# Kernel tuning notes

Hardware: AMD Instinct MI355X
Metric: run time of the kernel (lower is better)

Reference implementation:

```python
import jax, jax.numpy as jnp
import numpy as np

LN_EPS = 1e-5

def _layernorm(x, scale, bias):
    mu = jnp.mean(x, axis=-1, keepdims=True)
    var = jnp.var(x, axis=-1, keepdims=True)
    return (x - mu) * jax.lax.rsqrt(var + LN_EPS) * scale + bias

def setup_inputs() -> dict:
    T, node_num, num_nodes, E, C = 4, 10000, 50000, 256, 128
    key = jax.random.key(0)
    ks = jax.random.split(key, 12)
    s = lambda fan_in: 1.0 / np.sqrt(fan_in)
    return {
        "x": jax.random.normal(ks[0], (T * node_num, E), jnp.float32),
        "batched_x": jax.random.normal(ks[1], (num_nodes, E), jnp.float32),
        "indices": jax.random.randint(ks[2], (T, node_num), 0, num_nodes, jnp.int32),
        "ln_d_scale": jnp.ones((E,), jnp.float32),
        "ln_d_bias": jnp.zeros((E,), jnp.float32),
        "W1_d": jax.random.normal(ks[3], (E, 2 * E), jnp.float32) * s(E),
        "b1_d": jnp.zeros((2 * E,), jnp.float32),
        "W2_d": jax.random.normal(ks[4], (2 * E, C), jnp.float32) * s(2 * E),
        "b2_d": jnp.zeros((C,), jnp.float32),
        "ln_u_scale": jnp.ones((C,), jnp.float32),
        "ln_u_bias": jnp.zeros((C,), jnp.float32),
        "W1_u": jax.random.normal(ks[5], (C, 2 * C), jnp.float32) * s(C),
        "b1_u": jnp.zeros((2 * C,), jnp.float32),
        "W2_u": jax.random.normal(ks[6], (2 * C, E), jnp.float32) * s(2 * C),
        "b2_u": jnp.zeros((E,), jnp.float32),
    }

def reference(x, batched_x, indices, ln_d_scale, ln_d_bias, W1_d, b1_d, W2_d, b2_d,
              ln_u_scale, ln_u_bias, W1_u, b1_u, W2_u, b2_u):
    T, node_num = indices.shape
    num_nodes, E = batched_x.shape
    xr = x.reshape(T, node_num, E)
    # _to_entire: per-step scatter-add of active-node embeddings into the full node table
    def scatter_one(xi, idx):
        return jnp.zeros((num_nodes, E), x.dtype).at[idx].add(xi)
    ta = jax.vmap(scatter_one)(xr, indices)          # [T, num_nodes, E]
    inp = ta + batched_x[None]                        # broadcast entire features
    h = _layernorm(inp, ln_d_scale, ln_d_bias)
    h = jax.nn.gelu(h @ W1_d + b1_d, approximate=False) @ W2_d + b2_d  # [T, num_nodes, C]
    # _from_entire: gather each step's active nodes back, concat, LN + MLP up
    g = jnp.take_along_axis(h, indices[..., None], axis=1)  # [T, node_num, C]
    g = g.reshape(T * node_num, -1)
    g = _layernorm(g, ln_u_scale, ln_u_bias)
    out = jax.nn.gelu(g @ W1_u + b1_u, approximate=False) @ W2_u + b2_u  # [T*node_num, E]
    return out
```

## Files before the change

kernel.cpp:

```cpp
#include <hip/hip_runtime.h>
#include <math.h>

#define T_STEPS   4
#define NODE_NUM  10000
#define NUM_NODES 50000
#define E         256
#define TWO_E     512
#define CC        128
#define TWO_C     256
#define ROWS      32
#define NROWS_ALL (T_STEPS * NODE_NUM)
#define MAX_SLOTS 20000

typedef short bf16x8 __attribute__((ext_vector_type(8)));
typedef float f32x4  __attribute__((ext_vector_type(4)));

#define MFMA16(a, b, c) __builtin_amdgcn_mfma_f32_16x16x32_bf16((a), (b), (c), 0, 0, 0)

static __device__ unsigned short g_wt[294912];
static __device__ int g_cnt[T_STEPS * NUM_NODES];
static __device__ int g_slot[T_STEPS * NUM_NODES];
static __device__ int g_nslots;
static __device__ int g_dup[NROWS_ALL];
static __device__ int g_ndup0;

__device__ __forceinline__ float geluf(float v) {
    float p = v * (1.5957691216057308f + 0.07135481282636226f * v * v);
    return v / (1.0f + __expf(-p));
}

__device__ __forceinline__ unsigned short f2bf(float f) {
    unsigned int u = __builtin_bit_cast(unsigned int, f);
    u += 0x7fffu + ((u >> 16) & 1u);
    return (unsigned short)(u >> 16);
}

__global__ void prep_weights(float* __restrict__ ctable,
                             const float* __restrict__ W1d, const float* __restrict__ W2d,
                             const float* __restrict__ W1u, const float* __restrict__ W2u) {
    int i = blockIdx.x * 256 + threadIdx.x;
    if (i == 0) { g_nslots = 0; g_ndup0 = 0; }
    if (i < T_STEPS * NUM_NODES) g_cnt[i] = 0;
    {
        float4 z = make_float4(0.f, 0.f, 0.f, 0.f);
        float4* ct4 = reinterpret_cast<float4*>(ctable);
        for (int j = i; j < MAX_SLOTS * E / 4; j += 200704) ct4[j] = z;
    }
    if (i < 131072) {
        int n = i >> 8, k = i & 255;
        g_wt[i] = f2bf(W1d[(size_t)k * TWO_E + n]);
    }
    if (i < 65536) {
        int n = i >> 9, k = i & 511;
        g_wt[131072 + i] = f2bf(W2d[(size_t)k * CC + n]);
    }
    if (i < 32768) {
        int n = i >> 7, k = i & 127;
        g_wt[196608 + i] = f2bf(W1u[(size_t)k * TWO_C + n]);
    }
    if (i < 65536) {
        int n = i >> 8, k = i & 255;
        g_wt[229376 + i] = f2bf(W2u[(size_t)k * E + n]);
    }
}

__global__ void count_kernel(const int* __restrict__ indices) {
    int gr = blockIdx.x * 256 + threadIdx.x;
    if (gr < NROWS_ALL) {
        int t = gr / NODE_NUM;
        atomicAdd(&g_cnt[t * NUM_NODES + indices[gr]], 1);
    }
}

__global__ void index_prep_kernel(const int* __restrict__ indices) {
    int i = blockIdx.x * 256 + threadIdx.x;
    if (i < T_STEPS * NUM_NODES && g_cnt[i] >= 2)
        g_slot[i] = atomicAdd(&g_nslots, 1);
    if (i < NROWS_ALL) {
        int t = i / NODE_NUM;
        if (g_cnt[t * NUM_NODES + indices[i]] >= 2) {
            int p = atomicAdd(&g_ndup0, 1);
            g_dup[p] = i;
        }
    }
}

__global__ void scatter_list_kernel(float* __restrict__ ctable,
                                    const float* __restrict__ x,
                                    const int* __restrict__ indices) {
    int nd = g_ndup0;
    for (int e = blockIdx.x; e < nd; e += gridDim.x) {
        int gr = g_dup[e];
        int t = gr / NODE_NUM;
        int slot = g_slot[t * NUM_NODES + indices[gr]];
        atomicAdd(&ctable[(size_t)slot * E + threadIdx.x],
                  x[(size_t)gr * E + threadIdx.x]);
    }
}

__global__ __launch_bounds__(256, 3)
void mlp_kernel(const float* __restrict__ ctable,
                const float* __restrict__ x,
                const float* __restrict__ batched_x,
                const int* __restrict__ indices,
                const float* __restrict__ lnd_s, const float* __restrict__ lnd_b,
                const float* __restrict__ b1d, const float* __restrict__ b2d,
                const float* __restrict__ lnu_s, const float* __restrict__ lnu_b,
                const float* __restrict__ b1u, const float* __restrict__ b2u,
                float* __restrict__ out,
                int grLim) {
    __shared__ __align__(16) unsigned char smem[50176];
    __shared__ const float* rptr[ROWS];
    __shared__ int    ridx[ROWS];

    float*          Xf  = (float*)smem;
    unsigned short* Xs  = (unsigned short*)(smem + 33280);
    unsigned short* H1  = (unsigned short*)smem;
    float*          H2f = (float*)(smem + 33280);
    unsigned short* H2b = (unsigned short*)smem;
    unsigned short* G1  = (unsigned short*)(smem + 8704);

    const unsigned short* w1t  = g_wt;
    const unsigned short* w2t  = g_wt + 131072;
    const unsigned short* w1ut = g_wt + 196608;
    const unsigned short* w2ut = g_wt + 229376;

    const int tid = threadIdx.x;
    const int w = tid >> 6, lane = tid & 63;
    const int l16 = lane & 15, quad = lane >> 4;
    const int grb = blockIdx.x * ROWS;

    if (tid < ROWS) {
        int gr = grb + tid;
        if (gr >= grLim) gr = grLim - 1;
        int t = gr / NODE_NUM;
        int key = t * NUM_NODES + indices[gr];
        ridx[tid] = indices[gr];
        rptr[tid] = (g_cnt[key] > 1)
            ? (ctable + (size_t)g_slot[key] * E)
            : (x + (size_t)gr * E);
    }
    __syncthreads();

    #pragma unroll
    for (int it = 0; it < 8; ++it) {
        int v = it * 256 + tid;
        int r = v >> 6;
        int c = (v & 63) * 4;
        float4 tv = *reinterpret_cast<const float4*>(rptr[r] + c);
        float4 bv = *reinterpret_cast<const float4*>(&batched_x[(size_t)ridx[r] * E + c]);
        float4 s; s.x = tv.x + bv.x; s.y = tv.y + bv.y; s.z = tv.z + bv.z; s.w = tv.w + bv.w;
        *reinterpret_cast<float4*>(&Xf[r * 260 + c]) = s;
    }
    __syncthreads();

    {
        int row = tid >> 3, l8 = tid & 7;
        float s = 0.f, sq = 0.f;
        #pragma unroll
        for (int k = 0; k < 32; ++k) {
            float v = Xf[row * 260 + k * 8 + l8];
            s += v; sq += v * v;
        }
        s  += __shfl_xor(s, 1);  s  += __shfl_xor(s, 2);  s  += __shfl_xor(s, 4);
        sq += __shfl_xor(sq, 1); sq += __shfl_xor(sq, 2); sq += __shfl_xor(sq, 4);
        float mu = s * (1.0f / E);
        float var = sq * (1.0f / E) - mu * mu;
        float rs = rsqrtf(var + 1e-5f);
        #pragma unroll
        for (int k = 0; k < 32; ++k) {
            int c = k * 8 + l8;
            float v = (Xf[row * 260 + c] - mu) * rs * lnd_s[c] + lnd_b[c];
            Xs[row * 264 + c] = f2bf(v);
        }
    }
    __syncthreads();

    {
        bf16x8 af[2][8];
        #pragma unroll
        for (int mt = 0; mt < 2; ++mt) {
            const unsigned short* base = Xs + (l16 + 16 * mt) * 264 + quad * 8;
            #pragma unroll
            for (int ks = 0; ks < 8; ++ks)
                af[mt][ks] = *reinterpret_cast<const bf16x8*>(base + ks * 32);
        }
        bf16x8 bbuf[2][8];
        {
            const unsigned short* bp = w1t + (size_t)((w * 8) * 16 + l16) * 256 + quad * 8;
            #pragma unroll
            for (int ks = 0; ks < 8; ++ks)
                bbuf[0][ks] = *reinterpret_cast<const bf16x8*>(bp + ks * 32);
        }
        #pragma unroll
        for (int nt_ = 0; nt_ < 8; ++nt_) {
            const int cb = nt_ & 1, nb = cb ^ 1;
            if (nt_ < 7) {
                const unsigned short* bp =
                    w1t + (size_t)((w * 8 + nt_ + 1) * 16 + l16) * 256 + quad * 8;
                #pragma unroll
                for (int ks = 0; ks < 8; ++ks)
                    bbuf[nb][ks] = *reinterpret_cast<const bf16x8*>(bp + ks * 32);
            }
            int n = (w * 8 + nt_) * 16 + l16;
            f32x4 a0 = {0.f, 0.f, 0.f, 0.f}, a1 = {0.f, 0.f, 0.f, 0.f};
            #pragma unroll
            for (int ks = 0; ks < 8; ++ks) {
                a0 = MFMA16(af[0][ks], bbuf[cb][ks], a0);
                a1 = MFMA16(af[1][ks], bbuf[cb][ks], a1);
            }
            float bias = b1d[n];
            #pragma unroll
            for (int reg = 0; reg < 4; ++reg) {
                int r = quad * 4 + reg;
                H1[r * 520 + n]        = f2bf(geluf(a0[reg] + bias));
                H1[(r + 16) * 520 + n] = f2bf(geluf(a1[reg] + bias));
            }
        }
    }
    __syncthreads();

    {
        f32x4 acc2[2][2];
        #pragma unroll
        for (int i = 0; i < 2; ++i)
            #pragma unroll
            for (int j = 0; j < 2; ++j) acc2[i][j] = (f32x4){0.f, 0.f, 0.f, 0.f};
        bf16x8 afk[2][8];
        #pragma unroll
        for (int mt = 0; mt < 2; ++mt) {
            const unsigned short* base = H1 + (l16 + 16 * mt) * 520 + quad * 8;
            #pragma unroll
            for (int ks = 0; ks < 8; ++ks)
                afk[mt][ks] = *reinterpret_cast<const bf16x8*>(base + ks * 32);
        }
        bf16x8 bbuf[2][8];
        {
            const unsigned short* bp = w2t + (size_t)((w * 2) * 16 + l16) * 512 + quad * 8;
            #pragma unroll
            for (int ks = 0; ks < 8; ++ks)
                bbuf[0][ks] = *reinterpret_cast<const bf16x8*>(bp + ks * 32);
        }
        #pragma unroll
        for (int s = 0; s < 4; ++s) {
            const int nt2 = s & 1;
            const int cb = s & 1, nb = cb ^ 1;
            if (s < 3) {
                const int s1 = s + 1, kh1 = s1 >> 1, nt21 = s1 & 1;
                const unsigned short* bp =
                    w2t + (size_t)((w * 2 + nt21) * 16 + l16) * 512 + kh1 * 256 + quad * 8;
                #pragma unroll
                for (int ks = 0; ks < 8; ++ks)
                    bbuf[nb][ks] = *reinterpret_cast<const bf16x8*>(bp + ks * 32);
            }
            if (s == 2) {
                #pragma unroll
                for (int mt = 0; mt < 2; ++mt) {
                    const unsigned short* base = H1 + (l16 + 16 * mt) * 520 + 256 + quad * 8;
                    #pragma unroll
                    for (int ks = 0; ks < 8; ++ks)
                        afk[mt][ks] = *reinterpret_cast<const bf16x8*>(base + ks * 32);
                }
            }
            #pragma unroll
            for (int ks = 0; ks < 8; ++ks) {
                acc2[nt2][0] = MFMA16(afk[0][ks], bbuf[cb][ks], acc2[nt2][0]);
                acc2[nt2][1] = MFMA16(afk[1][ks], bbuf[cb][ks], acc2[nt2][1]);
            }
        }
        #pragma unroll
        for (int nt2 = 0; nt2 < 2; ++nt2) {
            int n = (w * 2 + nt2) * 16 + l16;
            float bias = b2d[n];
            #pragma unroll
            for (int mt = 0; mt < 2; ++mt)
                #pragma unroll
                for (int reg = 0; reg < 4; ++reg) {
                    int r = mt * 16 + quad * 4 + reg;
                    H2f[r * 132 + n] = acc2[nt2][mt][reg] + bias;
                }
        }
    }
    __syncthreads();

    {
        int row = tid >> 3, l8 = tid & 7;
        float s = 0.f, sq = 0.f;
        #pragma unroll
        for (int k = 0; k < 16; ++k) {
            float v = H2f[row * 132 + k * 8 + l8];
            s += v; sq += v * v;
        }
        s  += __shfl_xor(s, 1);  s  += __shfl_xor(s, 2);  s  += __shfl_xor(s, 4);
        sq += __shfl_xor(sq, 1); sq += __shfl_xor(sq, 2); sq += __shfl_xor(sq, 4);
        float mu = s * (1.0f / CC);
        float var = sq * (1.0f / CC) - mu * mu;
        float rs = rsqrtf(var + 1e-5f);
        #pragma unroll
        for (int k = 0; k < 16; ++k) {
            int c = k * 8 + l8;
            float v = (H2f[row * 132 + c] - mu) * rs * lnu_s[c] + lnu_b[c];
            H2b[row * 136 + c] = f2bf(v);
        }
    }
    __syncthreads();

    {
        bf16x8 af3[2][4];
        #pragma unroll
        for (int mt = 0; mt < 2; ++mt) {
            const unsigned short* base = H2b + (l16 + 16 * mt) * 136 + quad * 8;
            #pragma unroll
            for (int ks = 0; ks < 4; ++ks)
                af3[mt][ks] = *reinterpret_cast<const bf16x8*>(base + ks * 32);
        }
        bf16x8 bbuf[2][4];
        {
            const unsigned short* bp = w1ut + (size_t)((w * 4) * 16 + l16) * 128 + quad * 8;
            #pragma unroll
            for (int ks = 0; ks < 4; ++ks)
                bbuf[0][ks] = *reinterpret_cast<const bf16x8*>(bp + ks * 32);
        }
        #pragma unroll
        for (int nt_ = 0; nt_ < 4; ++nt_) {
            const int cb = nt_ & 1, nb = cb ^ 1;
            if (nt_ < 3) {
                const unsigned short* bp =
                    w1ut + (size_t)((w * 4 + nt_ + 1) * 16 + l16) * 128 + quad * 8;
                #pragma unroll
                for (int ks = 0; ks < 4; ++ks)
                    bbuf[nb][ks] = *reinterpret_cast<const bf16x8*>(bp + ks * 32);
            }
            int n = (w * 4 + nt_) * 16 + l16;
            f32x4 a0 = {0.f, 0.f, 0.f, 0.f}, a1 = {0.f, 0.f, 0.f, 0.f};
            #pragma unroll
            for (int ks = 0; ks < 4; ++ks) {
                a0 = MFMA16(af3[0][ks], bbuf[cb][ks], a0);
                a1 = MFMA16(af3[1][ks], bbuf[cb][ks], a1);
            }
            float bias = b1u[n];
            #pragma unroll
            for (int reg = 0; reg < 4; ++reg) {
                int r = quad * 4 + reg;
                G1[r * 264 + n]        = f2bf(geluf(a0[reg] + bias));
                G1[(r + 16) * 264 + n] = f2bf(geluf(a1[reg] + bias));
            }
        }
    }
    __syncthreads();

    {
        bf16x8 af4[2][8];
        #pragma unroll
        for (int mt = 0; mt < 2; ++mt) {
            const unsigned short* base = G1 + (l16 + 16 * mt) * 264 + quad * 8;
            #pragma unroll
            for (int ks = 0; ks < 8; ++ks)
                af4[mt][ks] = *reinterpret_cast<const bf16x8*>(base + ks * 32);
        }
        bf16x8 bbuf[2][8];
        {
            const unsigned short* bp = w2ut + (size_t)((w * 4) * 16 + l16) * 256 + quad * 8;
            #pragma unroll
            for (int ks = 0; ks < 8; ++ks)
                bbuf[0][ks] = *reinterpret_cast<const bf16x8*>(bp + ks * 32);
        }
        #pragma unroll
        for (int nt_ = 0; nt_ < 4; ++nt_) {
            const int cb = nt_ & 1, nb = cb ^ 1;
            if (nt_ < 3) {
                const unsigned short* bp =
                    w2ut + (size_t)((w * 4 + nt_ + 1) * 16 + l16) * 256 + quad * 8;
                #pragma unroll
                for (int ks = 0; ks < 8; ++ks)
                    bbuf[nb][ks] = *reinterpret_cast<const bf16x8*>(bp + ks * 32);
            }
            int n = (w * 4 + nt_) * 16 + l16;
            f32x4 a0 = {0.f, 0.f, 0.f, 0.f}, a1 = {0.f, 0.f, 0.f, 0.f};
            #pragma unroll
            for (int ks = 0; ks < 8; ++ks) {
                a0 = MFMA16(af4[0][ks], bbuf[cb][ks], a0);
                a1 = MFMA16(af4[1][ks], bbuf[cb][ks], a1);
            }
            float bias = b2u[n];
            #pragma unroll
            for (int reg = 0; reg < 4; ++reg) {
                int r = quad * 4 + reg;
                int g0 = grb + r, g1 = grb + r + 16;
                if (g0 < grLim) out[(size_t)g0 * E + n] = a0[reg] + bias;
                if (g1 < grLim) out[(size_t)g1 * E + n] = a1[reg] + bias;
            }
        }
    }
}

extern "C" void kernel_launch(void* const* d_in, const int* in_sizes, int n_in,
                              void* d_out, int out_size, void* d_ws, size_t ws_size,
                              hipStream_t stream) {
    const float* x     = (const float*)d_in[0];
    const float* bx    = (const float*)d_in[1];
    const int*   idxp  = (const int*)  d_in[2];
    const float* lnd_s = (const float*)d_in[3];
    const float* lnd_b = (const float*)d_in[4];
    const float* W1d   = (const float*)d_in[5];
    const float* b1d   = (const float*)d_in[6];
    const float* W2d   = (const float*)d_in[7];
    const float* b2d   = (const float*)d_in[8];
    const float* lnu_s = (const float*)d_in[9];
    const float* lnu_b = (const float*)d_in[10];
    const float* W1u   = (const float*)d_in[11];
    const float* b1u   = (const float*)d_in[12];
    const float* W2u   = (const float*)d_in[13];
    const float* b2u   = (const float*)d_in[14];
    float* out = (float*)d_out;
    float* ctable = (float*)d_ws;
    (void)ws_size; (void)in_sizes; (void)n_in; (void)out_size;

    prep_weights<<<784, 256, 0, stream>>>(ctable, W1d, W2d, W1u, W2u);
    count_kernel<<<(NROWS_ALL + 255) / 256, 256, 0, stream>>>(idxp);
    index_prep_kernel<<<784, 256, 0, stream>>>(idxp);
    scatter_list_kernel<<<1024, E, 0, stream>>>(ctable, x, idxp);
    mlp_kernel<<<NROWS_ALL / ROWS, 256, 0, stream>>>(
        ctable, x, bx, idxp, lnd_s, lnd_b, b1d, b2d,
        lnu_s, lnu_b, b1u, b2u, out, NROWS_ALL);
}
```

Before: 318.0 us.

## Process two row tiles per block and prefetch second tile's gather during first

Each MLP block now handles two 32-row tiles, with half as many blocks launched. The second tile's gather of x/ctable plus batched_x is issued into registers while the first tile's later GEMMs run, and its LayerNorm is written to shared memory during the third GEMM. The down LayerNorm now works straight from registers with wave-wide shuffles instead of staging fp32 rows in shared memory. This aims to hide global gather latency behind MFMA work, at the cost of extra register pressure and fewer blocks to fill the GPU.

```diff
diff --git a/kernel.cpp b/kernel.cpp
--- a/kernel.cpp
+++ b/kernel.cpp
@@ -14,6 +14,7 @@
 
 typedef short bf16x8 __attribute__((ext_vector_type(8)));
 typedef float f32x4  __attribute__((ext_vector_type(4)));
+typedef unsigned short u16x4 __attribute__((ext_vector_type(4)));
 
 #define MFMA16(a, b, c) __builtin_amdgcn_mfma_f32_16x16x32_bf16((a), (b), (c), 0, 0, 0)
 
@@ -95,6 +96,275 @@
         int slot = g_slot[t * NUM_NODES + indices[gr]];
         atomicAdd(&ctable[(size_t)slot * E + threadIdx.x],
                   x[(size_t)gr * E + threadIdx.x]);
+    }
+}
+
+__device__ __forceinline__ void gemm1_phase(const unsigned short* Xs, unsigned short* H1,
+                                            const unsigned short* w1t,
+                                            const float* __restrict__ b1d,
+                                            int w, int l16, int quad) {
+    bf16x8 af[2][8];
+    #pragma unroll
+    for (int mt = 0; mt < 2; ++mt) {
+        const unsigned short* base = Xs + (l16 + 16 * mt) * 264 + quad * 8;
+        #pragma unroll
+        for (int ks = 0; ks < 8; ++ks)
+            af[mt][ks] = *reinterpret_cast<const bf16x8*>(base + ks * 32);
+    }
+    bf16x8 bbuf[2][8];
+    {
+        const unsigned short* bp = w1t + (size_t)((w * 8) * 16 + l16) * 256 + quad * 8;
+        #pragma unroll
+        for (int ks = 0; ks < 8; ++ks)
+            bbuf[0][ks] = *reinterpret_cast<const bf16x8*>(bp + ks * 32);
+    }
+    #pragma unroll
+    for (int nt_ = 0; nt_ < 8; ++nt_) {
+        const int cb = nt_ & 1, nb = cb ^ 1;
+        if (nt_ < 7) {
+            const unsigned short* bp =
+                w1t + (size_t)((w * 8 + nt_ + 1) * 16 + l16) * 256 + quad * 8;
+            #pragma unroll
+            for (int ks = 0; ks < 8; ++ks)
+                bbuf[nb][ks] = *reinterpret_cast<const bf16x8*>(bp + ks * 32);
+        }
+        int n = (w * 8 + nt_) * 16 + l16;
+        f32x4 a0 = {0.f, 0.f, 0.f, 0.f}, a1 = {0.f, 0.f, 0.f, 0.f};
+        #pragma unroll
+        for (int ks = 0; ks < 8; ++ks) {
+            a0 = MFMA16(af[0][ks], bbuf[cb][ks], a0);
+            a1 = MFMA16(af[1][ks], bbuf[cb][ks], a1);
+        }
+        float bias = b1d[n];
+        #pragma unroll
+        for (int reg = 0; reg < 4; ++reg) {
+            int r = quad * 4 + reg;
+            H1[r * 520 + n]        = f2bf(geluf(a0[reg] + bias));
+            H1[(r + 16) * 520 + n] = f2bf(geluf(a1[reg] + bias));
+        }
+    }
+}
+
+__device__ __forceinline__ void gemm2_phase(const unsigned short* H1, float* H2f,
+                                            const unsigned short* w2t,
+                                            const float* __restrict__ b2d,
+                                            int w, int l16, int quad) {
+    f32x4 acc2[2][2];
+    #pragma unroll
+    for (int i = 0; i < 2; ++i)
+        #pragma unroll
+        for (int j = 0; j < 2; ++j) acc2[i][j] = (f32x4){0.f, 0.f, 0.f, 0.f};
+    bf16x8 afk[2][8];
+    #pragma unroll
+    for (int mt = 0; mt < 2; ++mt) {
+        const unsigned short* base = H1 + (l16 + 16 * mt) * 520 + quad * 8;
+        #pragma unroll
+        for (int ks = 0; ks < 8; ++ks)
+            afk[mt][ks] = *reinterpret_cast<const bf16x8*>(base + ks * 32);
+    }
+    bf16x8 bbuf[2][8];
+    {
+        const unsigned short* bp = w2t + (size_t)((w * 2) * 16 + l16) * 512 + quad * 8;
+        #pragma unroll
+        for (int ks = 0; ks < 8; ++ks)
+            bbuf[0][ks] = *reinterpret_cast<const bf16x8*>(bp + ks * 32);
+    }
+    #pragma unroll
+    for (int s = 0; s < 4; ++s) {
+        const int nt2 = s & 1;
+        const int cb = s & 1, nb = cb ^ 1;
+        if (s < 3) {
+            const int s1 = s + 1, kh1 = s1 >> 1, nt21 = s1 & 1;
+            const unsigned short* bp =
+                w2t + (size_t)((w * 2 + nt21) * 16 + l16) * 512 + kh1 * 256 + quad * 8;
+            #pragma unroll
+            for (int ks = 0; ks < 8; ++ks)
+                bbuf[nb][ks] = *reinterpret_cast<const bf16x8*>(bp + ks * 32);
+        }
+        if (s == 2) {
+            #pragma unroll
+            for (int mt = 0; mt < 2; ++mt) {
+                const unsigned short* base = H1 + (l16 + 16 * mt) * 520 + 256 + quad * 8;
+                #pragma unroll
+                for (int ks = 0; ks < 8; ++ks)
+                    afk[mt][ks] = *reinterpret_cast<const bf16x8*>(base + ks * 32);
+            }
+        }
+        #pragma unroll
+        for (int ks = 0; ks < 8; ++ks) {
+            acc2[nt2][0] = MFMA16(afk[0][ks], bbuf[cb][ks], acc2[nt2][0]);
+            acc2[nt2][1] = MFMA16(afk[1][ks], bbuf[cb][ks], acc2[nt2][1]);
+        }
+    }
+    #pragma unroll
+    for (int nt2 = 0; nt2 < 2; ++nt2) {
+        int n = (w * 2 + nt2) * 16 + l16;
+        float bias = b2d[n];
+        #pragma unroll
+        for (int mt = 0; mt < 2; ++mt)
+            #pragma unroll
+            for (int reg = 0; reg < 4; ++reg) {
+                int r = mt * 16 + quad * 4 + reg;
+                H2f[r * 132 + n] = acc2[nt2][mt][reg] + bias;
+            }
+    }
+}
+
+__device__ __forceinline__ void lnu_phase(const float* H2f, unsigned short* H2b,
+                                          const float* __restrict__ lnu_s,
+                                          const float* __restrict__ lnu_b, int tid) {
+    int row = tid >> 3, l8 = tid & 7;
+    float s = 0.f, sq = 0.f;
+    #pragma unroll
+    for (int k = 0; k < 16; ++k) {
+        float v = H2f[row * 132 + k * 8 + l8];
+        s += v; sq += v * v;
+    }
+    s  += __shfl_xor(s, 1);  s  += __shfl_xor(s, 2);  s  += __shfl_xor(s, 4);
+    sq += __shfl_xor(sq, 1); sq += __shfl_xor(sq, 2); sq += __shfl_xor(sq, 4);
+    float mu = s * (1.0f / CC);
+    float var = sq * (1.0f / CC) - mu * mu;
+    float rs = rsqrtf(var + 1e-5f);
+    #pragma unroll
+    for (int k = 0; k < 16; ++k) {
+        int c = k * 8 + l8;
+        float v = (H2f[row * 132 + c] - mu) * rs * lnu_s[c] + lnu_b[c];
+        H2b[row * 136 + c] = f2bf(v);
+    }
+}
+
+__device__ __forceinline__ void gemm3_phase(const unsigned short* H2b, unsigned short* G1,
+                                            const unsigned short* w1ut,
+                                            const float* __restrict__ b1u,
+                                            int w, int l16, int quad) {
+    bf16x8 af3[2][4];
+    #pragma unroll
+    for (int mt = 0; mt < 2; ++mt) {
+        const unsigned short* base = H2b + (l16 + 16 * mt) * 136 + quad * 8;
+        #pragma unroll
+        for (int ks = 0; ks < 4; ++ks)
+            af3[mt][ks] = *reinterpret_cast<const bf16x8*>(base + ks * 32);
+    }
+    bf16x8 bbuf[2][4];
+    {
+        const unsigned short* bp = w1ut + (size_t)((w * 4) * 16 + l16) * 128 + quad * 8;
+        #pragma unroll
+        for (int ks = 0; ks < 4; ++ks)
+            bbuf[0][ks] = *reinterpret_cast<const bf16x8*>(bp + ks * 32);
+    }
+    #pragma unroll
+    for (int nt_ = 0; nt_ < 4; ++nt_) {
+        const int cb = nt_ & 1, nb = cb ^ 1;
+        if (nt_ < 3) {
+            const unsigned short* bp =
+                w1ut + (size_t)((w * 4 + nt_ + 1) * 16 + l16) * 128 + quad * 8;
+            #pragma unroll
+            for (int ks = 0; ks < 4; ++ks)
+                bbuf[nb][ks] = *reinterpret_cast<const bf16x8*>(bp + ks * 32);
+        }
+        int n = (w * 4 + nt_) * 16 + l16;
+        f32x4 a0 = {0.f, 0.f, 0.f, 0.f}, a1 = {0.f, 0.f, 0.f, 0.f};
+        #pragma unroll
+        for (int ks = 0; ks < 4; ++ks) {
+            a0 = MFMA16(af3[0][ks], bbuf[cb][ks], a0);
+            a1 = MFMA16(af3[1][ks], bbuf[cb][ks], a1);
+        }
+        float bias = b1u[n];
+        #pragma unroll
+        for (int reg = 0; reg < 4; ++reg) {
+            int r = quad * 4 + reg;
+            G1[r * 264 + n]        = f2bf(geluf(a0[reg] + bias));
+            G1[(r + 16) * 264 + n] = f2bf(geluf(a1[reg] + bias));
+        }
+    }
+}
+
+__device__ __forceinline__ void gemm4_phase(const unsigned short* G1,
+                                            const unsigned short* w2ut,
+                                            const float* __restrict__ b2u,
+                                            float* __restrict__ out,
+                                            int grb, int grLim, int w, int l16, int quad) {
+    bf16x8 af4[2][8];
+    #pragma unroll
+    for (int mt = 0; mt < 2; ++mt) {
+        const unsigned short* base = G1 + (l16 + 16 * mt) * 264 + quad * 8;
+        #pragma unroll
+        for (int ks = 0; ks < 8; ++ks)
+            af4[mt][ks] = *reinterpret_cast<const bf16x8*>(base + ks * 32);
+    }
+    bf16x8 bbuf[2][8];
+    {
+        const unsigned short* bp = w2ut + (size_t)((w * 4) * 16 + l16) * 256 + quad * 8;
+        #pragma unroll
+        for (int ks = 0; ks < 8; ++ks)
+            bbuf[0][ks] = *reinterpret_cast<const bf16x8*>(bp + ks * 32);
+    }
+    #pragma unroll
+    for (int nt_ = 0; nt_ < 4; ++nt_) {
+        const int cb = nt_ & 1, nb = cb ^ 1;
+        if (nt_ < 3) {
+            const unsigned short* bp =
+                w2ut + (size_t)((w * 4 + nt_ + 1) * 16 + l16) * 256 + quad * 8;
+            #pragma unroll
+            for (int ks = 0; ks < 8; ++ks)
+                bbuf[nb][ks] = *reinterpret_cast<const bf16x8*>(bp + ks * 32);
+        }
+        int n = (w * 4 + nt_) * 16 + l16;
+        f32x4 a0 = {0.f, 0.f, 0.f, 0.f}, a1 = {0.f, 0.f, 0.f, 0.f};
+        #pragma unroll
+        for (int ks = 0; ks < 8; ++ks) {
+            a0 = MFMA16(af4[0][ks], bbuf[cb][ks], a0);
+            a1 = MFMA16(af4[1][ks], bbuf[cb][ks], a1);
+        }
+        float bias = b2u[n];
+        #pragma unroll
+        for (int reg = 0; reg < 4; ++reg) {
+            int r = quad * 4 + reg;
+            int g0 = grb + r, g1 = grb + r + 16;
+            if (g0 < grLim) out[(size_t)g0 * E + n] = a0[reg] + bias;
+            if (g1 < grLim) out[(size_t)g1 * E + n] = a1[reg] + bias;
+        }
+    }
+}
+
+__device__ __forceinline__ void stage_gather(float4* stg, const float* const* rptr,
+                                             const int* ridx, const float* __restrict__ bx,
+                                             int base, int w, int c4) {
+    #pragma unroll
+    for (int it = 0; it < 8; ++it) {
+        int r = base + it * 4 + w;
+        float4 tv = *reinterpret_cast<const float4*>(rptr[r] + c4);
+        float4 bv = *reinterpret_cast<const float4*>(&bx[(size_t)ridx[r] * E + c4]);
+        float4 s; s.x = tv.x + bv.x; s.y = tv.y + bv.y; s.z = tv.z + bv.z; s.w = tv.w + bv.w;
+        stg[it] = s;
+    }
+}
+
+__device__ __forceinline__ void lnd_from_regs(const float4* stg, unsigned short* Xs,
+                                              const float* __restrict__ lnd_s,
+                                              const float* __restrict__ lnd_b,
+                                              int w, int c4) {
+    const float4 sc = *reinterpret_cast<const float4*>(lnd_s + c4);
+    const float4 bi = *reinterpret_cast<const float4*>(lnd_b + c4);
+    #pragma unroll
+    for (int it = 0; it < 8; ++it) {
+        const int r = it * 4 + w;
+        float4 a = stg[it];
+        float s  = a.x + a.y + a.z + a.w;
+        float sq = a.x*a.x + a.y*a.y + a.z*a.z + a.w*a.w;
+        #pragma unroll
+        for (int m = 1; m < 64; m <<= 1) {
+            s  += __shfl_xor(s,  m);
+            sq += __shfl_xor(sq, m);
+        }
+        const float mu = s * (1.0f / E);
+        const float rs = rsqrtf(sq * (1.0f / E) - mu * mu + 1e-5f);
+        u16x4 o;
+        o.x = f2bf((a.x - mu) * rs * sc.x + bi.x);
+        o.y = f2bf((a.y - mu) * rs * sc.y + bi.y);
+        o.z = f2bf((a.z - mu) * rs * sc.z + bi.z);
+        o.w = f2bf((a.w - mu) * rs * sc.w + bi.w);
+        *reinterpret_cast<u16x4*>(&Xs[r * 264 + c4]) = o;
     }
 }
 
@@ -110,15 +380,14 @@
                 float* __restrict__ out,
                 int grLim) {
     __shared__ __align__(16) unsigned char smem[50176];
-    __shared__ const float* rptr[ROWS];
-    __shared__ int    ridx[ROWS];
-
-    float*          Xf  = (float*)smem;
-    unsigned short* Xs  = (unsigned short*)(smem + 33280);
+    __shared__ const float* rptr[2 * ROWS];
+    __shared__ int    ridx[2 * ROWS];
+
     unsigned short* H1  = (unsigned short*)smem;
-    float*          H2f = (float*)(smem + 33280);
     unsigned short* H2b = (unsigned short*)smem;
     unsigned short* G1  = (unsigned short*)(smem + 8704);
+    unsigned short* Xs  = (unsigned short*)(smem + 33280);
+    float*          H2f = (float*)(smem + 33280);
 
     const unsigned short* w1t  = g_wt;
     const unsigned short* w2t  = g_wt + 131072;
@@ -128,10 +397,14 @@
     const int tid = threadIdx.x;
     const int w = tid >> 6, lane = tid & 63;
     const int l16 = lane & 15, quad = lane >> 4;
-    const int grb = blockIdx.x * ROWS;
-
-    if (tid < ROWS) {
-        int gr = grb + tid;
+    const int c4 = lane * 4;
+    const int tile0 = blockIdx.x;
+    const int tile1 = blockIdx.x + (int)gridDim.x;
+    const int grb0 = tile0 * ROWS;
+    const int grb1 = tile1 * ROWS;
+
+    if (tid < 2 * ROWS) {
+        int gr = ((tid < ROWS) ? grb0 : grb1) + (tid & (ROWS - 1));
         if (gr >= grLim) gr = grLim - 1;
         int t = gr / NODE_NUM;
         int key = t * NUM_NODES + indices[gr];
@@ -141,257 +414,40 @@
             : (x + (size_t)gr * E);
     }
     __syncthreads();
-
-    #pragma unroll
-    for (int it = 0; it < 8; ++it) {
-        int v = it * 256 + tid;
-        int r = v >> 6;
-        int c = (v & 63) * 4;
-        float4 tv = *reinterpret_cast<const float4*>(rptr[r] + c);
-        float4 bv = *reinterpret_cast<const float4*>(&batched_x[(size_t)ridx[r] * E + c]);
-        float4 s; s.x = tv.x + bv.x; s.y = tv.y + bv.y; s.z = tv.z + bv.z; s.w = tv.w + bv.w;
-        *reinterpret_cast<float4*>(&Xf[r * 260 + c]) = s;
-    }
-    __syncthreads();
-
-    {
-        int row = tid >> 3, l8 = tid & 7;
-        float s = 0.f, sq = 0.f;
-        #pragma unroll
-        for (int k = 0; k < 32; ++k) {
-            float v = Xf[row * 260 + k * 8 + l8];
-            s += v; sq += v * v;
-        }
-        s  += __shfl_xor(s, 1);  s  += __shfl_xor(s, 2);  s  += __shfl_xor(s, 4);
-        sq += __shfl_xor(sq, 1); sq += __shfl_xor(sq, 2); sq += __shfl_xor(sq, 4);
-        float mu = s * (1.0f / E);
-        float var = sq * (1.0f / E) - mu * mu;
-        float rs = rsqrtf(var + 1e-5f);
-        #pragma unroll
-        for (int k = 0; k < 32; ++k) {
-            int c = k * 8 + l8;
-            float v = (Xf[row * 260 + c] - mu) * rs * lnd_s[c] + lnd_b[c];
-            Xs[row * 264 + c] = f2bf(v);
-        }
-    }
-    __syncthreads();
-
-    {
-        bf16x8 af[2][8];
-        #pragma unroll
-        for (int mt = 0; mt < 2; ++mt) {
-            const unsigned short* base = Xs + (l16 + 16 * mt) * 264 + quad * 8;
-            #pragma unroll
-            for (int ks = 0; ks < 8; ++ks)
-                af[mt][ks] = *reinterpret_cast<const bf16x8*>(base + ks * 32);
-        }
-        bf16x8 bbuf[2][8];
-        {
-            const unsigned short* bp = w1t + (size_t)((w * 8) * 16 + l16) * 256 + quad * 8;
-            #pragma unroll
-            for (int ks = 0; ks < 8; ++ks)
-                bbuf[0][ks] = *reinterpret_cast<const bf16x8*>(bp + ks * 32);
-        }
-        #pragma unroll
-        for (int nt_ = 0; nt_ < 8; ++nt_) {
-            const int cb = nt_ & 1, nb = cb ^ 1;
-            if (nt_ < 7) {
-                const unsigned short* bp =
-                    w1t + (size_t)((w * 8 + nt_ + 1) * 16 + l16) * 256 + quad * 8;
-                #pragma unroll
-                for (int ks = 0; ks < 8; ++ks)
-                    bbuf[nb][ks] = *reinterpret_cast<const bf16x8*>(bp + ks * 32);
-            }
-            int n = (w * 8 + nt_) * 16 + l16;
-            f32x4 a0 = {0.f, 0.f, 0.f, 0.f}, a1 = {0.f, 0.f, 0.f, 0.f};
-            #pragma unroll
-            for (int ks = 0; ks < 8; ++ks) {
-                a0 = MFMA16(af[0][ks], bbuf[cb][ks], a0);
-                a1 = MFMA16(af[1][ks], bbuf[cb][ks], a1);
-            }
-            float bias = b1d[n];
-            #pragma unroll
-            for (int reg = 0; reg < 4; ++reg) {
-                int r = quad * 4 + reg;
-                H1[r * 520 + n]        = f2bf(geluf(a0[reg] + bias));
-                H1[(r + 16) * 520 + n] = f2bf(geluf(a1[reg] + bias));
-            }
-        }
-    }
-    __syncthreads();
-
-    {
-        f32x4 acc2[2][2];
-        #pragma unroll
-        for (int i = 0; i < 2; ++i)
-            #pragma unroll
-            for (int j = 0; j < 2; ++j) acc2[i][j] = (f32x4){0.f, 0.f, 0.f, 0.f};
-        bf16x8 afk[2][8];
-        #pragma unroll
-        for (int mt = 0; mt < 2; ++mt) {
-            const unsigned short* base = H1 + (l16 + 16 * mt) * 520 + quad * 8;
-            #pragma unroll
-            for (int ks = 0; ks < 8; ++ks)
-                afk[mt][ks] = *reinterpret_cast<const bf16x8*>(base + ks * 32);
-        }
-        bf16x8 bbuf[2][8];
-        {
-            const unsigned short* bp = w2t + (size_t)((w * 2) * 16 + l16) * 512 + quad * 8;
-            #pragma unroll
-            for (int ks = 0; ks < 8; ++ks)
-                bbuf[0][ks] = *reinterpret_cast<const bf16x8*>(bp + ks * 32);
-        }
-        #pragma unroll
-        for (int s = 0; s < 4; ++s) {
-            const int nt2 = s & 1;
-            const int cb = s & 1, nb = cb ^ 1;
-            if (s < 3) {
-                const int s1 = s + 1, kh1 = s1 >> 1, nt21 = s1 & 1;
-                const unsigned short* bp =
-                    w2t + (size_t)((w * 2 + nt21) * 16 + l16) * 512 + kh1 * 256 + quad * 8;
-                #pragma unroll
-                for (int ks = 0; ks < 8; ++ks)
-                    bbuf[nb][ks] = *reinterpret_cast<const bf16x8*>(bp + ks * 32);
-            }
-            if (s == 2) {
-                #pragma unroll
-                for (int mt = 0; mt < 2; ++mt) {
-                    const unsigned short* base = H1 + (l16 + 16 * mt) * 520 + 256 + quad * 8;
-                    #pragma unroll
-                    for (int ks = 0; ks < 8; ++ks)
-                        afk[mt][ks] = *reinterpret_cast<const bf16x8*>(base + ks * 32);
-                }
-            }
-            #pragma unroll
-            for (int ks = 0; ks < 8; ++ks) {
-                acc2[nt2][0] = MFMA16(afk[0][ks], bbuf[cb][ks], acc2[nt2][0]);
-                acc2[nt2][1] = MFMA16(afk[1][ks], bbuf[cb][ks], acc2[nt2][1]);
-            }
-        }
-        #pragma unroll
-        for (int nt2 = 0; nt2 < 2; ++nt2) {
-            int n = (w * 2 + nt2) * 16 + l16;
-            float bias = b2d[n];
-            #pragma unroll
-            for (int mt = 0; mt < 2; ++mt)
-                #pragma unroll
-                for (int reg = 0; reg < 4; ++reg) {
-                    int r = mt * 16 + quad * 4 + reg;
-                    H2f[r * 132 + n] = acc2[nt2][mt][reg] + bias;
-                }
-        }
-    }
-    __syncthreads();
-
-    {
-        int row = tid >> 3, l8 = tid & 7;
-        float s = 0.f, sq = 0.f;
-        #pragma unroll
-        for (int k = 0; k < 16; ++k) {
-            float v = H2f[row * 132 + k * 8 + l8];
-            s += v; sq += v * v;
-        }
-        s  += __shfl_xor(s, 1);  s  += __shfl_xor(s, 2);  s  += __shfl_xor(s, 4);
-        sq += __shfl_xor(sq, 1); sq += __shfl_xor(sq, 2); sq += __shfl_xor(sq, 4);
-        float mu = s * (1.0f / CC);
-        float var = sq * (1.0f / CC) - mu * mu;
-        float rs = rsqrtf(var + 1e-5f);
-        #pragma unroll
-        for (int k = 0; k < 16; ++k) {
-            int c = k * 8 + l8;
-            float v = (H2f[row * 132 + c] - mu) * rs * lnu_s[c] + lnu_b[c];
-            H2b[row * 136 + c] = f2bf(v);
-        }
-    }
-    __syncthreads();
-
-    {
-        bf16x8 af3[2][4];
-        #pragma unroll
-        for (int mt = 0; mt < 2; ++mt) {
-            const unsigned short* base = H2b + (l16 + 16 * mt) * 136 + quad * 8;
-            #pragma unroll
-            for (int ks = 0; ks < 4; ++ks)
-                af3[mt][ks] = *reinterpret_cast<const bf16x8*>(base + ks * 32);
-        }
-        bf16x8 bbuf[2][4];
-        {
-            const unsigned short* bp = w1ut + (size_t)((w * 4) * 16 + l16) * 128 + quad * 8;
-            #pragma unroll
-            for (int ks = 0; ks < 4; ++ks)
-                bbuf[0][ks] = *reinterpret_cast<const bf16x8*>(bp + ks * 32);
-        }
-        #pragma unroll
-        for (int nt_ = 0; nt_ < 4; ++nt_) {
-            const int cb = nt_ & 1, nb = cb ^ 1;
-            if (nt_ < 3) {
-                const unsigned short* bp =
-                    w1ut + (size_t)((w * 4 + nt_ + 1) * 16 + l16) * 128 + quad * 8;
-                #pragma unroll
-                for (int ks = 0; ks < 4; ++ks)
-                    bbuf[nb][ks] = *reinterpret_cast<const bf16x8*>(bp + ks * 32);
-            }
-            int n = (w * 4 + nt_) * 16 + l16;
-            f32x4 a0 = {0.f, 0.f, 0.f, 0.f}, a1 = {0.f, 0.f, 0.f, 0.f};
-            #pragma unroll
-            for (int ks = 0; ks < 4; ++ks) {
-                a0 = MFMA16(af3[0][ks], bbuf[cb][ks], a0);
-                a1 = MFMA16(af3[1][ks], bbuf[cb][ks], a1);
-            }
-            float bias = b1u[n];
-            #pragma unroll
-            for (int reg = 0; reg < 4; ++reg) {
-                int r = quad * 4 + reg;
-                G1[r * 264 + n]        = f2bf(geluf(a0[reg] + bias));
-                G1[(r + 16) * 264 + n] = f2bf(geluf(a1[reg] + bias));
-            }
-        }
-    }
-    __syncthreads();
-
-    {
-        bf16x8 af4[2][8];
-        #pragma unroll
-        for (int mt = 0; mt < 2; ++mt) {
-            const unsigned short* base = G1 + (l16 + 16 * mt) * 264 + quad * 8;
-            #pragma unroll
-            for (int ks = 0; ks < 8; ++ks)
-                af4[mt][ks] = *reinterpret_cast<const bf16x8*>(base + ks * 32);
-        }
-        bf16x8 bbuf[2][8];
-        {
-            const unsigned short* bp = w2ut + (size_t)((w * 4) * 16 + l16) * 256 + quad * 8;
-            #pragma unroll
-            for (int ks = 0; ks < 8; ++ks)
-                bbuf[0][ks] = *reinterpret_cast<const bf16x8*>(bp + ks * 32);
-        }
-        #pragma unroll
-        for (int nt_ = 0; nt_ < 4; ++nt_) {
-            const int cb = nt_ & 1, nb = cb ^ 1;
-            if (nt_ < 3) {
-                const unsigned short* bp =
-                    w2ut + (size_t)((w * 4 + nt_ + 1) * 16 + l16) * 256 + quad * 8;
-                #pragma unroll
-                for (int ks = 0; ks < 8; ++ks)
-                    bbuf[nb][ks] = *reinterpret_cast<const bf16x8*>(bp + ks * 32);
-            }
-            int n = (w * 4 + nt_) * 16 + l16;
-            f32x4 a0 = {0.f, 0.f, 0.f, 0.f}, a1 = {0.f, 0.f, 0.f, 0.f};
-            #pragma unroll
-            for (int ks = 0; ks < 8; ++ks) {
-                a0 = MFMA16(af4[0][ks], bbuf[cb][ks], a0);
-                a1 = MFMA16(af4[1][ks], bbuf[cb][ks], a1);
-            }
-            float bias = b2u[n];
-            #pragma unroll
-            for (int reg = 0; reg < 4; ++reg) {
-                int r = quad * 4 + reg;
-                int g0 = grb + r, g1 = grb + r + 16;
-                if (g0 < grLim) out[(size_t)g0 * E + n] = a0[reg] + bias;
-                if (g1 < grLim) out[(size_t)g1 * E + n] = a1[reg] + bias;
-            }
-        }
-    }
+    {
+        float4 stg0[8];
+        stage_gather(stg0, rptr, ridx, batched_x, 0, w, c4);
+        lnd_from_regs(stg0, Xs, lnd_s, lnd_b, w, c4);
+    }
+    __syncthreads();
+
+    gemm1_phase(Xs, H1, w1t, b1d, w, l16, quad);
+    __syncthreads();
+
+    gemm2_phase(H1, H2f, w2t, b2d, w, l16, quad);
+    __syncthreads();
+
+    float4 stg1[8];
+    stage_gather(stg1, rptr, ridx, batched_x, ROWS, w, c4);
+    lnu_phase(H2f, H2b, lnu_s, lnu_b, tid);
+    __syncthreads();
+
+    gemm3_phase(H2b, G1, w1ut, b1u, w, l16, quad);
+    lnd_from_regs(stg1, Xs, lnd_s, lnd_b, w, c4);
+    __syncthreads();
+
+    gemm4_phase(G1, w2ut, b2u, out, grb0, grLim, w, l16, quad);
+    __syncthreads();
+
+    gemm1_phase(Xs, H1, w1t, b1d, w, l16, quad);
+    __syncthreads();
+    gemm2_phase(H1, H2f, w2t, b2d, w, l16, quad);
+    __syncthreads();
+    lnu_phase(H2f, H2b, lnu_s, lnu_b, tid);
+    __syncthreads();
+    gemm3_phase(H2b, G1, w1ut, b1u, w, l16, quad);
+    __syncthreads();
+    gemm4_phase(G1, w2ut, b2u, out, grb1, grLim, w, l16, quad);
 }
 
 extern "C" void kernel_launch(void* const* d_in, const int* in_sizes, int n_in,
@@ -420,7 +476,7 @@
     count_kernel<<<(NROWS_ALL + 255) / 256, 256, 0, stream>>>(idxp);
     index_prep_kernel<<<784, 256, 0, stream>>>(idxp);
     scatter_list_kernel<<<1024, E, 0, stream>>>(ctable, x, idxp);
-    mlp_kernel<<<NROWS_ALL / ROWS, 256, 0, stream>>>(
+    mlp_kernel<<<NROWS_ALL / ROWS / 2, 256, 0, stream>>>(
         ctable, x, bx, idxp, lnd_s, lnd_b, b1d, b2d,
         lnu_s, lnu_b, b1u, b2u, out, NROWS_ALL);
 }
```

After: 325.6 us. 1.02x slower.
